# Kernel optimization log

Measured on AMD Instinct MI355X. Metric: run time of the kernel, lower is better.

The kernel has to match this reference:

```python
import jax, jax.numpy as jnp
import numpy as np

B, L, D = 4, 2048, 512
DK = D // 2
DH = 256.0  # scaling denominator


def _skew(QE):
    # QE: [B, L, M] with M == L (relative position logits via skewing trick)
    b, l, m = QE.shape
    pad = jnp.zeros((b, l, 1), QE.dtype)
    cat = jnp.concatenate([pad, QE], axis=2)      # [B, L, M+1]
    reshaped = cat.reshape(b, m + 1, l)           # [B, M+1, L]
    return reshaped[:, 1:, :]                     # [B, M, L]


def setup_inputs() -> dict:
    key = jax.random.key(0)
    ks = jax.random.split(key, 7)
    return {
        "inputQ": jax.random.normal(ks[0], (B, L, D), jnp.float32),
        "inputK": jax.random.normal(ks[1], (B, L, D), jnp.float32),
        "inputV": jax.random.normal(ks[2], (B, L, D), jnp.float32),
        "Wq": jax.random.normal(ks[3], (D, DK), jnp.float32) * 0.02,
        "Wk": jax.random.normal(ks[4], (D, DK), jnp.float32) * 0.02,
        "Wv": jax.random.normal(ks[5], (D, D), jnp.float32) * 0.02,
        "E": jax.random.normal(ks[6], (L, DK), jnp.float32) * 0.02,
    }


def reference(inputQ, inputK, inputV, Wq, Wk, Wv, E):
    Q = jnp.einsum('bld,dk->blk', inputQ, Wq)   # [B, L, DK]
    K = jnp.einsum('bld,dk->blk', inputK, Wk)   # [B, L, DK]
    V = jnp.einsum('bld,de->ble', inputV, Wv)   # [B, L, D]
    QE = jnp.einsum('blk,mk->blm', Q, E)        # [B, L, max_seq]
    Srel = _skew(QE)                             # [B, L, L]
    QKt = jnp.einsum('blk,bmk->blm', Q, K)      # [B, L, L]
    attn = jax.nn.softmax((QKt + Srel) / jnp.sqrt(jnp.float32(DH)), axis=-1)
    return jnp.einsum('blm,bme->ble', attn, V)  # [B, L, D]
```

## Files before the change

kernel.cpp:

```cpp
#include <hip/hip_runtime.h>
#include <hip/hip_bf16.h>

#define BB 4
#define LL 2048
#define DD 512
#define DKK 256

typedef __bf16 bf16;
typedef __bf16 bf16x4 __attribute__((ext_vector_type(4)));
typedef __bf16 bf16x8 __attribute__((ext_vector_type(8)));
typedef float f32x4 __attribute__((ext_vector_type(4)));

__device__ __forceinline__ void async_ld16(const bf16* g, bf16* l) {
    __builtin_amdgcn_global_load_lds(
        (const __attribute__((address_space(1))) void*)g,
        (__attribute__((address_space(3))) void*)l, 16, 0, 0);
}

__global__ void conv3_f32_bf16(const float* __restrict__ a, const float* __restrict__ bq,
                               const float* __restrict__ c,
                               bf16* __restrict__ oa, bf16* __restrict__ ob,
                               bf16* __restrict__ oc, int n4) {
    const float* in = (blockIdx.y == 0) ? a : (blockIdx.y == 1) ? bq : c;
    bf16* out = (blockIdx.y == 0) ? oa : (blockIdx.y == 1) ? ob : oc;
    int i = blockIdx.x * 256 + threadIdx.x;
    if (i < n4) {
        f32x4 v = *(const f32x4*)(in + (size_t)i * 4);
        bf16x4 o;
        #pragma unroll
        for (int j = 0; j < 4; ++j) o[j] = (bf16)v[j];
        *(bf16x4*)(out + (size_t)i * 4) = o;
    }
}

__global__ void conv_f32_bf16v(const float* __restrict__ in, bf16* __restrict__ out, int n4) {
    int i = blockIdx.x * 256 + threadIdx.x;
    if (i < n4) {
        f32x4 v = *(const f32x4*)(in + (size_t)i * 4);
        bf16x4 o;
        #pragma unroll
        for (int j = 0; j < 4; ++j) o[j] = (bf16)v[j];
        *(bf16x4*)(out + (size_t)i * 4) = o;
    }
}

__global__ void transpose_f32_bf16(const float* __restrict__ in, bf16* __restrict__ out,
                                   int R, int C) {
    int idx = blockIdx.x * 256 + threadIdx.x;
    if (idx < R * C) {
        int r = idx / C, c = idx % C;
        out[(size_t)c * R + r] = (bf16)in[idx];
    }
}

__global__ void transpose_bf16_tile(const bf16* __restrict__ in, bf16* __restrict__ out,
                                    int R, int C) {
    __shared__ bf16 t[64][72];
    int tcx = C >> 6;
    int bx = blockIdx.x % tcx, by = blockIdx.x / tcx;
    int r = threadIdx.x >> 2, cc = (threadIdx.x & 3) * 16;
    const bf16* src = in + (size_t)(by * 64 + r) * C + bx * 64 + cc;
    bf16x8 v0 = *(const bf16x8*)src;
    bf16x8 v1 = *(const bf16x8*)(src + 8);
    #pragma unroll
    for (int u = 0; u < 8; ++u) { t[cc + u][r] = v0[u]; t[cc + 8 + u][r] = v1[u]; }
    __syncthreads();
    bf16* dst = out + (size_t)(bx * 64 + r) * R + by * 64 + cc;
    *(bf16x8*)dst = *(const bf16x8*)&t[r][cc];
    *(bf16x8*)(dst + 8) = *(const bf16x8*)&t[r][cc + 8];
}

template <int SKEW>
__launch_bounds__(256, 2)
__global__ void gemm128(const bf16* __restrict__ A, const bf16* __restrict__ B,
                        bf16* __restrict__ C, int N, int K,
                        long aStride, long bStride, long cStride)
{
    __shared__ bf16 Als[128 * 32];
    __shared__ bf16 Bls[128 * 32];

    int tid  = threadIdx.x;
    int lane = tid & 63;
    int wid  = tid >> 6;
    int l15  = lane & 15;
    int quad = lane >> 4;
    int nb = N >> 7;
    int gx = blockIdx.x % nb;
    int gy = blockIdx.x / nb;

    const bf16* Ab = A + (size_t)blockIdx.y * aStride + (size_t)gy * 128 * K;
    const bf16* Bb = B + (size_t)blockIdx.y * bStride + (size_t)gx * 128 * K;

    int rl = lane >> 2;
    int sl = lane & 3;
    int half = wid & 1;
    const bf16* gsrc = (wid < 2) ? Ab : Bb;
    bf16* ldst = (wid < 2) ? Als : Bls;

    f32x4 acc[4][4];
    #pragma unroll
    for (int i = 0; i < 4; ++i)
        #pragma unroll
        for (int j = 0; j < 4; ++j) acc[i][j] = 0;

    for (int k0 = 0; k0 < K; k0 += 32) {
        #pragma unroll
        for (int u = 0; u < 4; ++u) {
            int inst = half * 4 + u;
            int row  = inst * 16 + rl;
            int c    = (sl - (row >> 1)) & 3;
            async_ld16(gsrc + (size_t)row * K + k0 + c * 8, ldst + inst * 512);
        }
        __syncthreads();
        bf16x8 fA[4], fB[4];
        #pragma unroll
        for (int rt = 0; rt < 4; ++rt) {
            int row = (wid & 1) * 64 + rt * 16 + l15;
            int s   = (quad + (row >> 1)) & 3;
            fA[rt] = *(const bf16x8*)&Als[row * 32 + s * 8];
        }
        #pragma unroll
        for (int ct = 0; ct < 4; ++ct) {
            int col = (wid >> 1) * 64 + ct * 16 + l15;
            int s   = (quad + (col >> 1)) & 3;
            fB[ct] = *(const bf16x8*)&Bls[col * 32 + s * 8];
        }
        #pragma unroll
        for (int rt = 0; rt < 4; ++rt)
            #pragma unroll
            for (int ct = 0; ct < 4; ++ct)
                acc[rt][ct] = __builtin_amdgcn_mfma_f32_16x16x32_bf16(
                                  fA[rt], fB[ct], acc[rt][ct], 0, 0, 0);
        __syncthreads();
    }

    bf16* Cb = C + (size_t)blockIdx.y * cStride;
    int m0 = gy * 128 + (wid & 1) * 64;
    int n0 = gx * 128 + (wid >> 1) * 64;
    if (!SKEW) {
        #pragma unroll
        for (int rt = 0; rt < 4; ++rt)
            #pragma unroll
            for (int ct = 0; ct < 4; ++ct)
                #pragma unroll
                for (int r = 0; r < 4; ++r) {
                    int m = m0 + rt * 16 + quad * 4 + r;
                    int n = n0 + ct * 16 + l15;
                    Cb[(size_t)m * N + n] = (bf16)acc[rt][ct][r];
                }
    } else {
        #pragma unroll
        for (int rt = 0; rt < 4; ++rt)
            #pragma unroll
            for (int ct = 0; ct < 4; ++ct)
                #pragma unroll
                for (int r = 0; r < 4; ++r) {
                    int row = m0 + rt * 16 + quad * 4 + r;
                    int c   = n0 + ct * 16 + l15;
                    bool lower = (c >= LL - 1 - row);
                    int dr = lower ? row : row - 1;
                    int dc = lower ? c - (LL - 1 - row) : c + row + 1;
                    if (lower || row >= 1)
                        Cb[(size_t)dr * LL + dc] = (bf16)acc[rt][ct][r];
                }
    }
}

#define STAGE_K(JT) do {                                                        \
    _Pragma("unroll")                                                           \
    for (int u_ = 0; u_ < 8; ++u_) {                                            \
        int inst_ = wid * 8 + u_;                                               \
        int j_ = inst_ * 2 + (lane >> 5);                                       \
        int cp_ = lane & 31;                                                    \
        int c_ = (cp_ - j_) & 31;                                               \
        async_ld16(Kb + (size_t)((JT) + j_) * DKK + c_ * 8, Klds + inst_ * 512);\
    } } while (0)

#define STAGE_V(JT) do {                                                        \
    _Pragma("unroll")                                                           \
    for (int u_ = 0; u_ < 8; ++u_) {                                            \
        int inst_ = wid * 8 + u_;                                               \
        int d_ = inst_ * 8 + (lane >> 3);                                       \
        int cp_ = lane & 7;                                                     \
        int c_ = (cp_ - d_) & 7;                                                \
        async_ld16(Vb + (size_t)d_ * (BB * LL) + (JT) + c_ * 8,                 \
                   Vlds + inst_ * 512);                                         \
    } } while (0)

__launch_bounds__(256, 2)
__global__ void attn_kernel(const bf16* __restrict__ Qw, const bf16* __restrict__ Kw,
                            const bf16* __restrict__ Vt, const bf16* __restrict__ Srel,
                            float* __restrict__ out)
{
    __shared__ bf16  Klds[64 * 256];
    __shared__ bf16  Vlds[256 * 64];
    __shared__ float Ss[32][68];
    __shared__ bf16  Ps[32][72];
    __shared__ float mSt[32], lSt[32], aSt[32];

    int tid  = threadIdx.x;
    int lane = tid & 63;
    int wid  = tid >> 6;
    int l15  = lane & 15;
    int quad = lane >> 4;

    int xcd = blockIdx.x & 7;
    int b   = xcd >> 1;
    int dh  = xcd & 1;
    int i0  = (blockIdx.x >> 3) * 32;

    const bf16* Qb = Qw + (size_t)b * LL * DKK;
    const bf16* Kb = Kw + (size_t)b * LL * DKK;
    const bf16* Sb = Srel + (size_t)b * LL * LL;
    const bf16* Vb = Vt + (size_t)(dh * 256) * (BB * LL) + (size_t)b * LL;

    bf16x8 Qreg[2][8];
    #pragma unroll
    for (int rt = 0; rt < 2; ++rt)
        #pragma unroll
        for (int ks = 0; ks < 8; ++ks)
            Qreg[rt][ks] = *(const bf16x8*)(Qb + (size_t)(i0 + rt * 16 + l15) * DKK
                                            + ks * 32 + quad * 8);

    if (tid < 32) { mSt[tid] = -1e30f; lSt[tid] = 0.f; }

    f32x4 accO[2][4];
    #pragma unroll
    for (int rt = 0; rt < 2; ++rt)
        #pragma unroll
        for (int nt = 0; nt < 4; ++nt) accO[rt][nt] = 0;

    asm volatile("s_waitcnt vmcnt(0)" ::: "memory");

    STAGE_K(0);
    __builtin_amdgcn_sched_barrier(0);
    int srow = i0 + (tid >> 3), ssg = tid & 7;
    bf16x8 srelCur = *(const bf16x8*)(Sb + (size_t)srow * LL + ssg * 8);
    __builtin_amdgcn_sched_barrier(0);
    STAGE_V(0);

    for (int j0 = 0; j0 < LL; j0 += 64) {
        int jn = j0 + 64;
        bool notlast = (jn < LL);

        asm volatile("s_waitcnt vmcnt(9)" ::: "memory");
        bf16x8 kf[8];
        int jrow = wid * 16 + l15;
        #pragma unroll
        for (int ks = 0; ks < 8; ++ks) {
            int cp = (ks * 4 + quad + jrow) & 31;
            kf[ks] = *(const bf16x8*)&Klds[jrow * 256 + cp * 8];
        }
        asm volatile("s_waitcnt lgkmcnt(0)" ::: "memory");
        __builtin_amdgcn_sched_barrier(0);
        if (notlast) { STAGE_K(jn); }
        __builtin_amdgcn_sched_barrier(0);
        bf16x8 srelNext;
        if (notlast)
            srelNext = *(const bf16x8*)(Sb + (size_t)srow * LL + jn + ssg * 8);
        __builtin_amdgcn_sched_barrier(0);
        f32x4 s0 = 0, s1 = 0;
        __builtin_amdgcn_s_setprio(1);
        #pragma unroll
        for (int ks = 0; ks < 8; ++ks) {
            s0 = __builtin_amdgcn_mfma_f32_16x16x32_bf16(Qreg[0][ks], kf[ks], s0, 0, 0, 0);
            s1 = __builtin_amdgcn_mfma_f32_16x16x32_bf16(Qreg[1][ks], kf[ks], s1, 0, 0, 0);
        }
        __builtin_amdgcn_s_setprio(0);
        #pragma unroll
        for (int r = 0; r < 4; ++r) {
            Ss[quad * 4 + r][wid * 16 + l15]      = s0[r];
            Ss[16 + quad * 4 + r][wid * 16 + l15] = s1[r];
        }
        asm volatile("s_waitcnt lgkmcnt(0)\ns_barrier" ::: "memory");

        {
            int r = tid >> 3, sg = tid & 7;
            int i = i0 + r;
            float v[8];
            #pragma unroll
            for (int c = 0; c < 8; ++c) {
                float sr = (j0 + sg * 8 + c == i + 1) ? 0.f : (float)srelCur[c];
                v[c] = (Ss[r][sg * 8 + c] + sr) * 0.0625f;
            }
            float tmax = v[0];
            #pragma unroll
            for (int c = 1; c < 8; ++c) tmax = fmaxf(tmax, v[c]);
            tmax = fmaxf(tmax, __shfl_xor(tmax, 1));
            tmax = fmaxf(tmax, __shfl_xor(tmax, 2));
            tmax = fmaxf(tmax, __shfl_xor(tmax, 4));
            float mOld = mSt[r], lOld = lSt[r];
            float mNew = fmaxf(mOld, tmax);
            float alpha = __expf(mOld - mNew);
            float ps = 0.f;
            bf16x8 pv;
            #pragma unroll
            for (int c = 0; c < 8; ++c) {
                float p = __expf(v[c] - mNew);
                ps += p;
                pv[c] = (bf16)p;
            }
            ps += __shfl_xor(ps, 1);
            ps += __shfl_xor(ps, 2);
            ps += __shfl_xor(ps, 4);
            *(bf16x8*)&Ps[r][sg * 8] = pv;
            if (sg == 0) { mSt[r] = mNew; lSt[r] = alpha * lOld + ps; aSt[r] = alpha; }
        }
        srelCur = srelNext;
        asm volatile("s_waitcnt lgkmcnt(0)\ns_barrier" ::: "memory");

        if (notlast) asm volatile("s_waitcnt vmcnt(9)" ::: "memory");
        else         asm volatile("s_waitcnt vmcnt(0)" ::: "memory");
        bf16x8 aF[2][2];
        #pragma unroll
        for (int rt = 0; rt < 2; ++rt)
            #pragma unroll
            for (int kk = 0; kk < 2; ++kk)
                aF[rt][kk] = *(const bf16x8*)&Ps[rt * 16 + l15][kk * 32 + quad * 8];
        float ar[2][4];
        #pragma unroll
        for (int rt = 0; rt < 2; ++rt)
            #pragma unroll
            for (int r = 0; r < 4; ++r) ar[rt][r] = aSt[rt * 16 + quad * 4 + r];
        bf16x8 vf[4][2];
        #pragma unroll
        for (int nt = 0; nt < 4; ++nt) {
            int dd = wid * 64 + nt * 16 + l15;
            int c0 = (quad + dd) & 7;
            int c1 = (4 + quad + dd) & 7;
            vf[nt][0] = *(const bf16x8*)&Vlds[dd * 64 + c0 * 8];
            vf[nt][1] = *(const bf16x8*)&Vlds[dd * 64 + c1 * 8];
        }
        asm volatile("s_waitcnt lgkmcnt(0)" ::: "memory");
        __builtin_amdgcn_sched_barrier(0);
        if (notlast) { STAGE_V(jn); }
        __builtin_amdgcn_sched_barrier(0);
        __builtin_amdgcn_s_setprio(1);
        #pragma unroll
        for (int nt = 0; nt < 4; ++nt) {
            #pragma unroll
            for (int rt = 0; rt < 2; ++rt) {
                f32x4 o = accO[rt][nt];
                o[0] *= ar[rt][0]; o[1] *= ar[rt][1];
                o[2] *= ar[rt][2]; o[3] *= ar[rt][3];
                o = __builtin_amdgcn_mfma_f32_16x16x32_bf16(aF[rt][0], vf[nt][0], o, 0, 0, 0);
                o = __builtin_amdgcn_mfma_f32_16x16x32_bf16(aF[rt][1], vf[nt][1], o, 0, 0, 0);
                accO[rt][nt] = o;
            }
        }
        __builtin_amdgcn_s_setprio(0);
    }
    float lr[2][4];
    #pragma unroll
    for (int rt = 0; rt < 2; ++rt)
        #pragma unroll
        for (int r = 0; r < 4; ++r) lr[rt][r] = 1.f / lSt[rt * 16 + quad * 4 + r];
    #pragma unroll
    for (int rt = 0; rt < 2; ++rt)
        #pragma unroll
        for (int nt = 0; nt < 4; ++nt)
            #pragma unroll
            for (int r = 0; r < 4; ++r) {
                int i = i0 + rt * 16 + quad * 4 + r;
                int d = dh * 256 + wid * 64 + nt * 16 + l15;
                out[((size_t)b * LL + i) * DD + d] = accO[rt][nt][r] * lr[rt][r];
            }
}

extern "C" void kernel_launch(void* const* d_in, const int* in_sizes, int n_in,
                              void* d_out, int out_size, void* d_ws, size_t ws_size,
                              hipStream_t stream) {
    const float* inQ = (const float*)d_in[0];
    const float* inK = (const float*)d_in[1];
    const float* inV = (const float*)d_in[2];
    const float* Wq  = (const float*)d_in[3];
    const float* Wk  = (const float*)d_in[4];
    const float* Wv  = (const float*)d_in[5];
    const float* E   = (const float*)d_in[6];
    float* out = (float*)d_out;

    char* ws = (char*)d_ws;
    bf16* Qw   = (bf16*)(ws);
    bf16* Kw   = (bf16*)(ws + ((size_t)4  << 20));
    bf16* Vt   = (bf16*)(ws + ((size_t)8  << 20));
    bf16* SrelW= (bf16*)(ws + ((size_t)16 << 20));
    bf16* Xq   = (bf16*)(ws + ((size_t)16 << 20));
    bf16* Xk   = (bf16*)(ws + ((size_t)24 << 20));
    bf16* Xv   = (bf16*)(ws + ((size_t)32 << 20));
    bf16* Vw   = (bf16*)(ws + ((size_t)40 << 20));
    bf16* WqT  = (bf16*)(ws + ((size_t)48 << 20));
    bf16* WkT  = (bf16*)(ws + ((size_t)48 << 20) + 262144);
    bf16* WvT  = (bf16*)(ws + ((size_t)48 << 20) + 524288);
    bf16* Eb   = (bf16*)(ws + ((size_t)49 << 20));

    conv3_f32_bf16<<<dim3(4096, 3), 256, 0, stream>>>(inQ, inK, inV, Xq, Xk, Xv,
                                                      (BB * LL * DD) / 4);
    conv_f32_bf16v<<<512,  256, 0, stream>>>(E, Eb, (LL * DKK) / 4);
    transpose_f32_bf16<<<512,  256, 0, stream>>>(Wq, WqT, DD, DKK);
    transpose_f32_bf16<<<512,  256, 0, stream>>>(Wk, WkT, DD, DKK);
    transpose_f32_bf16<<<1024, 256, 0, stream>>>(Wv, WvT, DD, DD);

    gemm128<0><<<dim3(2 * 64, 2),  256, 0, stream>>>(Xq, WqT, Qw, DKK, DD,
                                                     4194304L, 131072L, 2097152L);
    gemm128<0><<<dim3(4 * 64, 1),  256, 0, stream>>>(Xv, WvT, Vw, DD, DD, 0, 0, 0);
    transpose_bf16_tile<<<(DD / 64) * (BB * LL / 64), 256, 0, stream>>>(Vw, Vt, BB * LL, DD);
    gemm128<1><<<dim3(16 * 16, BB), 256, 0, stream>>>(Qw, Eb, SrelW, LL, DKK,
                                                      (long)LL * DKK, 0, (long)LL * LL);
    attn_kernel<<<dim3(BB * 64 * 2), 256, 0, stream>>>(Qw, Kw, Vt, SrelW, out);
}
```

Measured before the change: 238.2 us.

## Load K and V fragments directly from global memory instead of LDS staging

```diff
diff --git a/kernel.cpp b/kernel.cpp
--- a/kernel.cpp
+++ b/kernel.cpp
@@ -166,34 +166,11 @@
     }
 }
 
-#define STAGE_K(JT) do {                                                        \
-    _Pragma("unroll")                                                           \
-    for (int u_ = 0; u_ < 8; ++u_) {                                            \
-        int inst_ = wid * 8 + u_;                                               \
-        int j_ = inst_ * 2 + (lane >> 5);                                       \
-        int cp_ = lane & 31;                                                    \
-        int c_ = (cp_ - j_) & 31;                                               \
-        async_ld16(Kb + (size_t)((JT) + j_) * DKK + c_ * 8, Klds + inst_ * 512);\
-    } } while (0)
-
-#define STAGE_V(JT) do {                                                        \
-    _Pragma("unroll")                                                           \
-    for (int u_ = 0; u_ < 8; ++u_) {                                            \
-        int inst_ = wid * 8 + u_;                                               \
-        int d_ = inst_ * 8 + (lane >> 3);                                       \
-        int cp_ = lane & 7;                                                     \
-        int c_ = (cp_ - d_) & 7;                                                \
-        async_ld16(Vb + (size_t)d_ * (BB * LL) + (JT) + c_ * 8,                 \
-                   Vlds + inst_ * 512);                                         \
-    } } while (0)
-
 __launch_bounds__(256, 2)
 __global__ void attn_kernel(const bf16* __restrict__ Qw, const bf16* __restrict__ Kw,
                             const bf16* __restrict__ Vt, const bf16* __restrict__ Srel,
                             float* __restrict__ out)
 {
-    __shared__ bf16  Klds[64 * 256];
-    __shared__ bf16  Vlds[256 * 64];
     __shared__ float Ss[32][68];
     __shared__ bf16  Ps[32][72];
     __shared__ float mSt[32], lSt[32], aSt[32];
@@ -230,35 +207,24 @@
         #pragma unroll
         for (int nt = 0; nt < 4; ++nt) accO[rt][nt] = 0;
 
-    asm volatile("s_waitcnt vmcnt(0)" ::: "memory");
-
-    STAGE_K(0);
-    __builtin_amdgcn_sched_barrier(0);
     int srow = i0 + (tid >> 3), ssg = tid & 7;
     bf16x8 srelCur = *(const bf16x8*)(Sb + (size_t)srow * LL + ssg * 8);
-    __builtin_amdgcn_sched_barrier(0);
-    STAGE_V(0);
+
+    int jrow = wid * 16 + l15;
 
     for (int j0 = 0; j0 < LL; j0 += 64) {
         int jn = j0 + 64;
         bool notlast = (jn < LL);
 
-        asm volatile("s_waitcnt vmcnt(9)" ::: "memory");
         bf16x8 kf[8];
-        int jrow = wid * 16 + l15;
-        #pragma unroll
-        for (int ks = 0; ks < 8; ++ks) {
-            int cp = (ks * 4 + quad + jrow) & 31;
-            kf[ks] = *(const bf16x8*)&Klds[jrow * 256 + cp * 8];
-        }
-        asm volatile("s_waitcnt lgkmcnt(0)" ::: "memory");
-        __builtin_amdgcn_sched_barrier(0);
-        if (notlast) { STAGE_K(jn); }
-        __builtin_amdgcn_sched_barrier(0);
-        bf16x8 srelNext;
+        const bf16* krow = Kb + (size_t)(j0 + jrow) * DKK;
+        #pragma unroll
+        for (int ks = 0; ks < 8; ++ks)
+            kf[ks] = *(const bf16x8*)(krow + ks * 32 + quad * 8);
+        bf16x8 srelNext = srelCur;
         if (notlast)
             srelNext = *(const bf16x8*)(Sb + (size_t)srow * LL + jn + ssg * 8);
-        __builtin_amdgcn_sched_barrier(0);
+
         f32x4 s0 = 0, s1 = 0;
         __builtin_amdgcn_s_setprio(1);
         #pragma unroll
@@ -272,6 +238,16 @@
             Ss[quad * 4 + r][wid * 16 + l15]      = s0[r];
             Ss[16 + quad * 4 + r][wid * 16 + l15] = s1[r];
         }
+
+        bf16x8 vf[4][2];
+        #pragma unroll
+        for (int nt = 0; nt < 4; ++nt) {
+            int dd = wid * 64 + nt * 16 + l15;
+            const bf16* vrow = Vb + (size_t)dd * (BB * LL) + j0;
+            vf[nt][0] = *(const bf16x8*)(vrow + quad * 8);
+            vf[nt][1] = *(const bf16x8*)(vrow + 32 + quad * 8);
+        }
+
         asm volatile("s_waitcnt lgkmcnt(0)\ns_barrier" ::: "memory");
 
         {
@@ -309,8 +285,6 @@
         srelCur = srelNext;
         asm volatile("s_waitcnt lgkmcnt(0)\ns_barrier" ::: "memory");
 
-        if (notlast) asm volatile("s_waitcnt vmcnt(9)" ::: "memory");
-        else         asm volatile("s_waitcnt vmcnt(0)" ::: "memory");
         bf16x8 aF[2][2];
         #pragma unroll
         for (int rt = 0; rt < 2; ++rt)
@@ -322,19 +296,6 @@
         for (int rt = 0; rt < 2; ++rt)
             #pragma unroll
             for (int r = 0; r < 4; ++r) ar[rt][r] = aSt[rt * 16 + quad * 4 + r];
-        bf16x8 vf[4][2];
-        #pragma unroll
-        for (int nt = 0; nt < 4; ++nt) {
-            int dd = wid * 64 + nt * 16 + l15;
-            int c0 = (quad + dd) & 7;
-            int c1 = (4 + quad + dd) & 7;
-            vf[nt][0] = *(const bf16x8*)&Vlds[dd * 64 + c0 * 8];
-            vf[nt][1] = *(const bf16x8*)&Vlds[dd * 64 + c1 * 8];
-        }
-        asm volatile("s_waitcnt lgkmcnt(0)" ::: "memory");
-        __builtin_amdgcn_sched_barrier(0);
-        if (notlast) { STAGE_V(jn); }
-        __builtin_amdgcn_sched_barrier(0);
         __builtin_amdgcn_s_setprio(1);
         #pragma unroll
         for (int nt = 0; nt < 4; ++nt) {
```

Result: slower. 285.2 us (+19.7%).
